# Performance work log

Hardware: AMD Instinct MI355X
Metric: run time of the kernel (lower is better)

Reference implementation:

```python
import jax, jax.numpy as jnp
import numpy as np

N_PDE = 4096
SENSOR_RANGE = 0.08
WINDOW = int(SENSOR_RANGE * N_PDE)   # 327
HALF = WINDOW // 2                   # 163
RESIZE_LEN = 20
FREQS = jnp.array([1.0, 2.0, 4.0, 8.0], dtype=jnp.float32)
EPS = 1e-6  # flax GroupNorm default epsilon
U_MAX, V_MAX = 40.0, 1.0
N_AGENTS = 262144


def setup_inputs() -> dict:
    key = jax.random.key(0)
    ks = jax.random.split(key, 16)

    def w(k, shape):
        fan_in = shape[0]
        return (jax.random.normal(k, shape, jnp.float32) / np.float32(np.sqrt(fan_in)))

    return {
        "z_curr": jax.random.normal(ks[0], (N_PDE,), jnp.float32),
        "z_target": jax.random.normal(ks[1], (N_PDE,), jnp.float32),
        "xi_curr": jax.random.uniform(ks[2], (N_AGENTS,), jnp.float32),
        # branch net (features=[256,256]), each layer: Dense + GroupNorm(1 group) + tanh
        "bW0": w(ks[3], (2 * RESIZE_LEN, 256)), "bb0": jnp.zeros((256,), jnp.float32),
        "bs0": jnp.ones((256,), jnp.float32), "bB0": jnp.zeros((256,), jnp.float32),
        "bW1": w(ks[4], (256, 256)), "bb1": jnp.zeros((256,), jnp.float32),
        "bs1": jnp.ones((256,), jnp.float32), "bB1": jnp.zeros((256,), jnp.float32),
        # trunk net: 8 -> 32 -> 32
        "tW0": w(ks[5], (8, 32)), "tb0": jnp.zeros((32,), jnp.float32),
        "tW1": w(ks[6], (32, 32)), "tb1": jnp.zeros((32,), jnp.float32),
        # combined head: (256+32) -> 32, then two 32 -> 1 heads
        "cW": w(ks[7], (256 + 32, 32)), "cb": jnp.zeros((32,), jnp.float32),
        "uW": w(ks[8], (32, 1)), "ub": jnp.zeros((1,), jnp.float32),
        "vW": w(ks[9], (32, 1)), "vb": jnp.zeros((1,), jnp.float32),
    }


def _local_obs(padded_error, xi):
    # per-agent dynamic slice + finite-difference gradient + bilinear resize
    center = (xi * (N_PDE - 1)).astype(jnp.int32) + HALF
    start = center - HALF
    p_err = jax.lax.dynamic_slice(padded_error, (start,), (WINDOW,))
    p_grad = jnp.gradient(p_err)
    p_err = jax.image.resize(p_err, (RESIZE_LEN,), method='bilinear')
    p_grad = jax.image.resize(p_grad, (RESIZE_LEN,), method='bilinear')
    return jnp.concatenate([p_err, p_grad])  # [40]


def _groupnorm1(x, scale, bias):
    # GroupNorm(num_groups=1) applied per-sample over the feature axis
    mu = jnp.mean(x, axis=-1, keepdims=True)
    var = jnp.var(x, axis=-1, keepdims=True)
    return (x - mu) * jax.lax.rsqrt(var + EPS) * scale + bias


def reference(z_curr, z_target, xi_curr,
              bW0, bb0, bs0, bB0, bW1, bb1, bs1, bB1,
              tW0, tb0, tW1, tb1, cW, cb, uW, ub, vW, vb):
    error = z_curr - z_target
    padded = jnp.pad(error, (HALF, HALF), mode='edge')  # [N_PDE + 2*HALF]

    patches = jax.vmap(lambda xi: _local_obs(padded, xi))(xi_curr)  # [A, 40]

    # branch net
    h = jnp.tanh(_groupnorm1(patches @ bW0 + bb0, bs0, bB0))  # [A, 256]
    h = jnp.tanh(_groupnorm1(h @ bW1 + bb1, bs1, bB1))        # [A, 256]

    # trunk net
    angle = xi_curr[:, None] * FREQS * jnp.pi                 # [A, 4]
    enc = jnp.concatenate([jnp.sin(angle), jnp.cos(angle)], axis=-1)  # [A, 8]
    enc = jnp.tanh(enc @ tW0 + tb0)
    enc = jnp.tanh(enc @ tW1 + tb1)                           # [A, 32]

    combined = jnp.concatenate([h, enc], axis=-1)             # [A, 288]
    x = jnp.tanh(combined @ cW + cb)                          # [A, 32]
    u_raw = (x @ uW + ub).squeeze(-1)
    v_raw = (x @ vW + vb).squeeze(-1)
    return (U_MAX * jnp.tanh(u_raw), V_MAX * jnp.tanh(v_raw))
```

## Files before the change

### kernel.cpp

```cpp
#include <hip/hip_runtime.h>

#define NP      4096
#define WINDOW  327
#define HALF    163
#define RL      20
#define NA      262144
#define GN_EPS  1e-6f
#define R       4
#define NBLK    (NP / R)
#define NT      512

__device__ __forceinline__ float tanh_fast(float x) {
  float e = __expf(2.0f * x);
  return 1.0f - 2.0f / (e + 1.0f);
}

__device__ __forceinline__ void wave_sum2(float& a, float& b) {
#pragma unroll
  for (int m = 1; m < 64; m <<= 1) {
    a += __shfl_xor(a, m, 64);
    b += __shfl_xor(b, m, 64);
  }
}

#define L_ESP   0
#define L_OBS   332
#define L_PART  0
#define L_HBUF  8192
#define L_HCL   9232
#define L_TOT   9376

__global__ __launch_bounds__(NT, 8) void dc_table(
    const float* __restrict__ zc,  const float* __restrict__ zt,
    const float* __restrict__ bW0, const float* __restrict__ bb0,
    const float* __restrict__ bs0, const float* __restrict__ bB0,
    const float* __restrict__ bW1, const float* __restrict__ bb1,
    const float* __restrict__ bs1, const float* __restrict__ bB1,
    const float* __restrict__ tW0, const float* __restrict__ tb0,
    const float* __restrict__ tW1, const float* __restrict__ tb1,
    const float* __restrict__ cW,  const float* __restrict__ cb,
    const float* __restrict__ uW,  const float* __restrict__ ub,
    const float* __restrict__ vW,  const float* __restrict__ vb,
    float* __restrict__ tbl)
{
  __shared__ __align__(16) float sm[L_TOT];
  float* espan = sm + L_ESP;
  float* obsT  = sm + L_OBS;
  float* part  = sm + L_PART;
  float* hbuf  = sm + L_HBUF;
  float* hcL   = sm + L_HCL;

  const int tid = threadIdx.x;
  const int w   = tid >> 6;
  const int l   = tid & 63;
  const int s0  = blockIdx.x * R;

  if (tid < WINDOW + R - 1) {
    int c = s0 - HALF + tid;
    c = c < 0 ? 0 : (c > NP - 1 ? NP - 1 : c);
    espan[tid] = zc[c] - zt[c];
  }
  __syncthreads();

  if (tid < R * 2 * RL) {
    const float INV  = (float)WINDOW / (float)RL;
    const float RINV = (float)RL / (float)WINDOW;
    int q = tid % (2 * RL);
    int r = tid / (2 * RL);
    int qq = (q < RL) ? q : q - RL;
    float xs = ((float)qq + 0.5f) * INV - 0.5f;
    int jlo = (int)ceilf(xs - INV);  if (jlo < 0) jlo = 0;
    int jhi = (int)floorf(xs + INV); if (jhi > WINDOW - 1) jhi = WINDOW - 1;
    const float* p = espan + r;
    float wsum = 0.0f, acc = 0.0f;
    for (int j = jlo; j <= jhi; ++j) {
      float wq = 1.0f - fabsf(xs - (float)j) * RINV;
      float v;
      if (q < RL) {
        v = p[j];
      } else {
        v = (j == 0) ? (p[1] - p[0]) :
            (j == WINDOW - 1) ? (p[WINDOW - 1] - p[WINDOW - 2]) :
            0.5f * (p[j + 1] - p[j - 1]);
      }
      wsum += wq;
      acc  += wq * v;
    }
    obsT[q * 4 + r] = acc / wsum;
  }
  __syncthreads();

  float acc[R][4];

#pragma unroll
  for (int r = 0; r < R; ++r) { acc[r][0]=0.f; acc[r][1]=0.f; acc[r][2]=0.f; acc[r][3]=0.f; }
  for (int kk = 0; kk < 5; ++kk) {
    int k = w * 5 + kk;
    float4 wt = *(const float4*)&bW0[k * 256 + 4 * l];
    float4 o  = *(const float4*)&obsT[k * 4];
    const float wv[4] = {wt.x, wt.y, wt.z, wt.w};
    const float ov[4] = {o.x, o.y, o.z, o.w};
#pragma unroll
    for (int r = 0; r < R; ++r)
#pragma unroll
      for (int j = 0; j < 4; ++j) acc[r][j] = fmaf(ov[r], wv[j], acc[r][j]);
  }
  __syncthreads();

#pragma unroll
  for (int r = 0; r < R; ++r)
    *(float4*)&part[w * 1024 + r * 256 + 4 * l] = make_float4(acc[r][0], acc[r][1], acc[r][2], acc[r][3]);
  __syncthreads();
  if (w < 4) {
    int rr = w, g = l;
    float4 b0 = *(const float4*)&bb0[4 * g];
    float val[4] = {b0.x, b0.y, b0.z, b0.w};
#pragma unroll
    for (int w2 = 0; w2 < 8; ++w2) {
      float4 p0 = *(const float4*)&part[w2 * 1024 + rr * 256 + 4 * g];
      val[0]+=p0.x; val[1]+=p0.y; val[2]+=p0.z; val[3]+=p0.w;
    }
    float s = 0.f, q = 0.f;
#pragma unroll
    for (int i = 0; i < 4; ++i) { s += val[i]; q += val[i] * val[i]; }
    wave_sum2(s, q);
    float mu  = s * (1.0f / 256.0f);
    float var = fmaxf(q * (1.0f / 256.0f) - mu * mu, 0.0f);
    float rv  = rsqrtf(var + GN_EPS);
    float4 sc0 = *(const float4*)&bs0[4 * g];
    float4 sh0 = *(const float4*)&bB0[4 * g];
    const float sc[4] = {sc0.x,sc0.y,sc0.z,sc0.w};
    const float sh[4] = {sh0.x,sh0.y,sh0.z,sh0.w};
    float h[4];
#pragma unroll
    for (int i = 0; i < 4; ++i) h[i] = tanh_fast((val[i] - mu) * rv * sc[i] + sh[i]);
    *(float4*)&hbuf[rr * 260 + 4 * g] = make_float4(h[0], h[1], h[2], h[3]);
  }
  __syncthreads();

#pragma unroll
  for (int r = 0; r < R; ++r) { acc[r][0]=0.f; acc[r][1]=0.f; acc[r][2]=0.f; acc[r][3]=0.f; }
  for (int kk = 0; kk < 32; kk += 4) {
    int k0 = w * 32 + kk;
    float4 wt0 = *(const float4*)&bW1[(k0    ) * 256 + 4 * l];
    float4 wt1 = *(const float4*)&bW1[(k0 + 1) * 256 + 4 * l];
    float4 wt2 = *(const float4*)&bW1[(k0 + 2) * 256 + 4 * l];
    float4 wt3 = *(const float4*)&bW1[(k0 + 3) * 256 + 4 * l];
    float4 hr[R];
#pragma unroll
    for (int r = 0; r < R; ++r) hr[r] = *(const float4*)&hbuf[r * 260 + k0];
#pragma unroll
    for (int r = 0; r < R; ++r) {
      const float* hp = (const float*)&hr[r];
      acc[r][0] = fmaf(hp[0], wt0.x, acc[r][0]); acc[r][1] = fmaf(hp[0], wt0.y, acc[r][1]);
      acc[r][2] = fmaf(hp[0], wt0.z, acc[r][2]); acc[r][3] = fmaf(hp[0], wt0.w, acc[r][3]);
      acc[r][0] = fmaf(hp[1], wt1.x, acc[r][0]); acc[r][1] = fmaf(hp[1], wt1.y, acc[r][1]);
      acc[r][2] = fmaf(hp[1], wt1.z, acc[r][2]); acc[r][3] = fmaf(hp[1], wt1.w, acc[r][3]);
      acc[r][0] = fmaf(hp[2], wt2.x, acc[r][0]); acc[r][1] = fmaf(hp[2], wt2.y, acc[r][1]);
      acc[r][2] = fmaf(hp[2], wt2.z, acc[r][2]); acc[r][3] = fmaf(hp[2], wt2.w, acc[r][3]);
      acc[r][0] = fmaf(hp[3], wt3.x, acc[r][0]); acc[r][1] = fmaf(hp[3], wt3.y, acc[r][1]);
      acc[r][2] = fmaf(hp[3], wt3.z, acc[r][2]); acc[r][3] = fmaf(hp[3], wt3.w, acc[r][3]);
    }
  }

#pragma unroll
  for (int r = 0; r < R; ++r)
    *(float4*)&part[w * 1024 + r * 256 + 4 * l] = make_float4(acc[r][0], acc[r][1], acc[r][2], acc[r][3]);
  __syncthreads();
  if (w < 4) {
    int rr = w, g = l;
    float4 b0 = *(const float4*)&bb1[4 * g];
    float val[4] = {b0.x, b0.y, b0.z, b0.w};
#pragma unroll
    for (int w2 = 0; w2 < 8; ++w2) {
      float4 p0 = *(const float4*)&part[w2 * 1024 + rr * 256 + 4 * g];
      val[0]+=p0.x; val[1]+=p0.y; val[2]+=p0.z; val[3]+=p0.w;
    }
    float s = 0.f, q = 0.f;
#pragma unroll
    for (int i = 0; i < 4; ++i) { s += val[i]; q += val[i] * val[i]; }
    wave_sum2(s, q);
    float mu  = s * (1.0f / 256.0f);
    float var = fmaxf(q * (1.0f / 256.0f) - mu * mu, 0.0f);
    float rv  = rsqrtf(var + GN_EPS);
    float4 sc0 = *(const float4*)&bs1[4 * g];
    float4 sh0 = *(const float4*)&bB1[4 * g];
    const float sc[4] = {sc0.x,sc0.y,sc0.z,sc0.w};
    const float sh[4] = {sh0.x,sh0.y,sh0.z,sh0.w};
    float h[4];
#pragma unroll
    for (int i = 0; i < 4; ++i) h[i] = tanh_fast((val[i] - mu) * rv * sc[i] + sh[i]);
    *(float4*)&hbuf[rr * 260 + 4 * g] = make_float4(h[0], h[1], h[2], h[3]);
  }
  __syncthreads();

  if (w < 4) {
    int r  = w;
    int kg = l >> 3;
    int c  = (l & 7) * 4;
    float ga0 = 0.f, ga1 = 0.f, ga2 = 0.f, ga3 = 0.f;
#pragma unroll
    for (int ii = 0; ii < 8; ++ii) {
      int j  = (ii + kg) & 7;
      int kb = kg * 32 + 4 * j;
      float4 hv = *(const float4*)&hbuf[r * 260 + kb];
      const float hvv[4] = {hv.x, hv.y, hv.z, hv.w};
#pragma unroll
      for (int i2 = 0; i2 < 4; ++i2) {
        float4 cw = *(const float4*)&cW[(kb + i2) * 32 + c];
        ga0 = fmaf(hvv[i2], cw.x, ga0);
        ga1 = fmaf(hvv[i2], cw.y, ga1);
        ga2 = fmaf(hvv[i2], cw.z, ga2);
        ga3 = fmaf(hvv[i2], cw.w, ga3);
      }
    }
#pragma unroll
    for (int m = 8; m < 64; m <<= 1) {
      ga0 += __shfl_xor(ga0, m, 64);
      ga1 += __shfl_xor(ga1, m, 64);
      ga2 += __shfl_xor(ga2, m, 64);
      ga3 += __shfl_xor(ga3, m, 64);
    }
    if (l < 8) {
      float4 cbv = *(const float4*)&cb[c];
      *(float4*)&hcL[r * 36 + c] = make_float4(ga0 + cbv.x, ga1 + cbv.y, ga2 + cbv.z, ga3 + cbv.w);
    }
  }
  __syncthreads();

  if (tid < 64) {
    int v = tid >> 3, sub = tid & 7;
    int r = v >> 1, e = v & 1;
    int jg = s0 + r + e;
    float xe = (float)jg * (1.0f / 4095.0f);
    float enc[8];
#pragma unroll
    for (int k = 0; k < 4; ++k) {
      float fr = (float)(1 << k);
      float a = (xe * fr) * 3.14159265358979f;
      enc[k]     = sinf(a);
      enc[k + 4] = cosf(a);
    }
    int base = tid & ~7;

    float t0v[4];
#pragma unroll
    for (int i = 0; i < 4; ++i) {
      int f = 4 * sub + i;
      float a = tb0[f];
#pragma unroll
      for (int k = 0; k < 8; ++k) a = fmaf(enc[k], tW0[k * 32 + f], a);
      t0v[i] = tanh_fast(a);
    }

    float t1v[4];
#pragma unroll
    for (int i = 0; i < 4; ++i) t1v[i] = tb1[4 * sub + i];
#pragma unroll
    for (int j8 = 0; j8 < 8; ++j8) {
#pragma unroll
      for (int i2 = 0; i2 < 4; ++i2) {
        float tv = __shfl(t0v[i2], base + j8, 64);
        int k = 4 * j8 + i2;
#pragma unroll
        for (int i = 0; i < 4; ++i) t1v[i] = fmaf(tv, tW1[k * 32 + 4 * sub + i], t1v[i]);
      }
    }
#pragma unroll
    for (int i = 0; i < 4; ++i) t1v[i] = tanh_fast(t1v[i]);

    float xvv[4];
#pragma unroll
    for (int i = 0; i < 4; ++i) xvv[i] = hcL[r * 36 + 4 * sub + i];
#pragma unroll
    for (int j8 = 0; j8 < 8; ++j8) {
#pragma unroll
      for (int i2 = 0; i2 < 4; ++i2) {
        float tv = __shfl(t1v[i2], base + j8, 64);
        int k = 4 * j8 + i2;
#pragma unroll
        for (int i = 0; i < 4; ++i) xvv[i] = fmaf(tv, cW[(256 + k) * 32 + 4 * sub + i], xvv[i]);
      }
    }
#pragma unroll
    for (int i = 0; i < 4; ++i) xvv[i] = tanh_fast(xvv[i]);

    float up = 0.f, vp = 0.f;
#pragma unroll
    for (int i = 0; i < 4; ++i) {
      up = fmaf(xvv[i], uW[4 * sub + i], up);
      vp = fmaf(xvv[i], vW[4 * sub + i], vp);
    }
#pragma unroll
    for (int m = 1; m < 8; m <<= 1) {
      up += __shfl_xor(up, m, 64);
      vp += __shfl_xor(vp, m, 64);
    }
    if (sub == 0) {
      int s = s0 + r;
      tbl[4 * s + e]     = 40.0f * tanh_fast(up + ub[0]);
      tbl[4 * s + 2 + e] = tanh_fast(vp + vb[0]);
    }
  }
}

__global__ __launch_bounds__(256) void dc_agents(
    const float* __restrict__ xi_curr, const float4* __restrict__ tbl,
    float* __restrict__ out)
{
  int a = blockIdx.x * 256 + threadIdx.x;
  float xi = xi_curr[a];
  float p = xi * 4095.0f;
  int s = (int)p;
  s = s > 4095 ? 4095 : s;
  float t = p - (float)s;
  float4 tb = tbl[s];
  out[a]      = fmaf(t, tb.y - tb.x, tb.x);
  out[NA + a] = fmaf(t, tb.w - tb.z, tb.z);
}

extern "C" void kernel_launch(void* const* d_in, const int* in_sizes, int n_in,
                              void* d_out, int out_size, void* d_ws, size_t ws_size,
                              hipStream_t stream) {
  const float* zc  = (const float*)d_in[0];
  const float* zt  = (const float*)d_in[1];
  const float* xi  = (const float*)d_in[2];
  const float* bW0 = (const float*)d_in[3];
  const float* bb0 = (const float*)d_in[4];
  const float* bs0 = (const float*)d_in[5];
  const float* bB0 = (const float*)d_in[6];
  const float* bW1 = (const float*)d_in[7];
  const float* bb1 = (const float*)d_in[8];
  const float* bs1 = (const float*)d_in[9];
  const float* bB1 = (const float*)d_in[10];
  const float* tW0 = (const float*)d_in[11];
  const float* tb0 = (const float*)d_in[12];
  const float* tW1 = (const float*)d_in[13];
  const float* tb1 = (const float*)d_in[14];
  const float* cW  = (const float*)d_in[15];
  const float* cb  = (const float*)d_in[16];
  const float* uW  = (const float*)d_in[17];
  const float* ub  = (const float*)d_in[18];
  const float* vW  = (const float*)d_in[19];
  const float* vb  = (const float*)d_in[20];

  float* tbl = (float*)d_ws;
  float* out = (float*)d_out;

  dc_table<<<NBLK, NT, 0, stream>>>(zc, zt, bW0, bb0, bs0, bB0,
                                    bW1, bb1, bs1, bB1,
                                    tW0, tb0, tW1, tb1, cW, cb,
                                    uW, ub, vW, vb, tbl);
  dc_agents<<<NA / 256, 256, 0, stream>>>(xi, (const float4*)tbl, out);
}
```

Before: 146.0 us.

## Process eight table rows per block with 256 threads to improve weight reuse

Doubles the rows handled per block from four to eight and halves the block size to four waves. Each loaded weight vector of the branch-net layers is now reused across eight rows, and the cross-wave reduction is done in two passes of four rows through a smaller shared buffer. The grid halves to 512 blocks, trading block count and register pressure (eight-row accumulators, launch bound of 3) for fewer global weight loads per row.

```diff
diff --git a/kernel.cpp b/kernel.cpp
--- a/kernel.cpp
+++ b/kernel.cpp
@@ -6,9 +6,9 @@
 #define RL      20
 #define NA      262144
 #define GN_EPS  1e-6f
-#define R       4
+#define R       8
 #define NBLK    (NP / R)
-#define NT      512
+#define NT      256
 
 __device__ __forceinline__ float tanh_fast(float x) {
   float e = __expf(2.0f * x);
@@ -24,13 +24,13 @@
 }
 
 #define L_ESP   0
-#define L_OBS   332
+#define L_OBS   336
 #define L_PART  0
-#define L_HBUF  8192
-#define L_HCL   9232
-#define L_TOT   9376
-
-__global__ __launch_bounds__(NT, 8) void dc_table(
+#define L_HBUF  4096
+#define L_HCL   6176
+#define L_TOT   6464
+
+__global__ __launch_bounds__(NT, 3) void dc_table(
     const float* __restrict__ zc,  const float* __restrict__ zt,
     const float* __restrict__ bW0, const float* __restrict__ bb0,
     const float* __restrict__ bs0, const float* __restrict__ bB0,
@@ -55,38 +55,40 @@
   const int l   = tid & 63;
   const int s0  = blockIdx.x * R;
 
-  if (tid < WINDOW + R - 1) {
-    int c = s0 - HALF + tid;
+  for (int t = tid; t < WINDOW + R - 1; t += NT) {
+    int c = s0 - HALF + t;
     c = c < 0 ? 0 : (c > NP - 1 ? NP - 1 : c);
-    espan[tid] = zc[c] - zt[c];
+    espan[t] = zc[c] - zt[c];
   }
   __syncthreads();
 
-  if (tid < R * 2 * RL) {
+  {
     const float INV  = (float)WINDOW / (float)RL;
     const float RINV = (float)RL / (float)WINDOW;
-    int q = tid % (2 * RL);
-    int r = tid / (2 * RL);
-    int qq = (q < RL) ? q : q - RL;
-    float xs = ((float)qq + 0.5f) * INV - 0.5f;
-    int jlo = (int)ceilf(xs - INV);  if (jlo < 0) jlo = 0;
-    int jhi = (int)floorf(xs + INV); if (jhi > WINDOW - 1) jhi = WINDOW - 1;
-    const float* p = espan + r;
-    float wsum = 0.0f, acc = 0.0f;
-    for (int j = jlo; j <= jhi; ++j) {
-      float wq = 1.0f - fabsf(xs - (float)j) * RINV;
-      float v;
-      if (q < RL) {
-        v = p[j];
-      } else {
-        v = (j == 0) ? (p[1] - p[0]) :
-            (j == WINDOW - 1) ? (p[WINDOW - 1] - p[WINDOW - 2]) :
-            0.5f * (p[j + 1] - p[j - 1]);
-      }
-      wsum += wq;
-      acc  += wq * v;
-    }
-    obsT[q * 4 + r] = acc / wsum;
+    for (int task = tid; task < R * 2 * RL; task += NT) {
+      int q = task % (2 * RL);
+      int r = task / (2 * RL);
+      int qq = (q < RL) ? q : q - RL;
+      float xs = ((float)qq + 0.5f) * INV - 0.5f;
+      int jlo = (int)ceilf(xs - INV);  if (jlo < 0) jlo = 0;
+      int jhi = (int)floorf(xs + INV); if (jhi > WINDOW - 1) jhi = WINDOW - 1;
+      const float* p = espan + r;
+      float wsum = 0.0f, acc = 0.0f;
+      for (int j = jlo; j <= jhi; ++j) {
+        float wq = 1.0f - fabsf(xs - (float)j) * RINV;
+        float v;
+        if (q < RL) {
+          v = p[j];
+        } else {
+          v = (j == 0) ? (p[1] - p[0]) :
+              (j == WINDOW - 1) ? (p[WINDOW - 1] - p[WINDOW - 2]) :
+              0.5f * (p[j + 1] - p[j - 1]);
+        }
+        wsum += wq;
+        acc  += wq * v;
+      }
+      obsT[q * 8 + r] = acc / wsum;
+    }
   }
   __syncthreads();
 
@@ -94,12 +96,13 @@
 
 #pragma unroll
   for (int r = 0; r < R; ++r) { acc[r][0]=0.f; acc[r][1]=0.f; acc[r][2]=0.f; acc[r][3]=0.f; }
-  for (int kk = 0; kk < 5; ++kk) {
-    int k = w * 5 + kk;
+  for (int kk = 0; kk < 10; ++kk) {
+    int k = w * 10 + kk;
     float4 wt = *(const float4*)&bW0[k * 256 + 4 * l];
-    float4 o  = *(const float4*)&obsT[k * 4];
+    float4 o0 = *(const float4*)&obsT[k * 8];
+    float4 o1 = *(const float4*)&obsT[k * 8 + 4];
     const float wv[4] = {wt.x, wt.y, wt.z, wt.w};
-    const float ov[4] = {o.x, o.y, o.z, o.w};
+    const float ov[8] = {o0.x, o0.y, o0.z, o0.w, o1.x, o1.y, o1.z, o1.w};
 #pragma unroll
     for (int r = 0; r < R; ++r)
 #pragma unroll
@@ -108,94 +111,106 @@
   __syncthreads();
 
 #pragma unroll
-  for (int r = 0; r < R; ++r)
-    *(float4*)&part[w * 1024 + r * 256 + 4 * l] = make_float4(acc[r][0], acc[r][1], acc[r][2], acc[r][3]);
-  __syncthreads();
-  if (w < 4) {
-    int rr = w, g = l;
-    float4 b0 = *(const float4*)&bb0[4 * g];
-    float val[4] = {b0.x, b0.y, b0.z, b0.w};
-#pragma unroll
-    for (int w2 = 0; w2 < 8; ++w2) {
-      float4 p0 = *(const float4*)&part[w2 * 1024 + rr * 256 + 4 * g];
-      val[0]+=p0.x; val[1]+=p0.y; val[2]+=p0.z; val[3]+=p0.w;
-    }
-    float s = 0.f, q = 0.f;
-#pragma unroll
-    for (int i = 0; i < 4; ++i) { s += val[i]; q += val[i] * val[i]; }
-    wave_sum2(s, q);
-    float mu  = s * (1.0f / 256.0f);
-    float var = fmaxf(q * (1.0f / 256.0f) - mu * mu, 0.0f);
-    float rv  = rsqrtf(var + GN_EPS);
-    float4 sc0 = *(const float4*)&bs0[4 * g];
-    float4 sh0 = *(const float4*)&bB0[4 * g];
-    const float sc[4] = {sc0.x,sc0.y,sc0.z,sc0.w};
-    const float sh[4] = {sh0.x,sh0.y,sh0.z,sh0.w};
-    float h[4];
-#pragma unroll
-    for (int i = 0; i < 4; ++i) h[i] = tanh_fast((val[i] - mu) * rv * sc[i] + sh[i]);
-    *(float4*)&hbuf[rr * 260 + 4 * g] = make_float4(h[0], h[1], h[2], h[3]);
-  }
-  __syncthreads();
+  for (int p = 0; p < 2; ++p) {
+#pragma unroll
+    for (int r = 0; r < 4; ++r)
+      *(float4*)&part[w * 1024 + r * 256 + 4 * l] =
+        make_float4(acc[4*p+r][0], acc[4*p+r][1], acc[4*p+r][2], acc[4*p+r][3]);
+    __syncthreads();
+    {
+      int row = 4 * p + w;
+      float4 b0 = *(const float4*)&bb0[4 * l];
+      float val[4] = {b0.x, b0.y, b0.z, b0.w};
+#pragma unroll
+      for (int w2 = 0; w2 < 4; ++w2) {
+        float4 p0 = *(const float4*)&part[w2 * 1024 + w * 256 + 4 * l];
+        val[0]+=p0.x; val[1]+=p0.y; val[2]+=p0.z; val[3]+=p0.w;
+      }
+      float s = 0.f, q = 0.f;
+#pragma unroll
+      for (int i = 0; i < 4; ++i) { s += val[i]; q += val[i] * val[i]; }
+      wave_sum2(s, q);
+      float mu  = s * (1.0f / 256.0f);
+      float var = fmaxf(q * (1.0f / 256.0f) - mu * mu, 0.0f);
+      float rv  = rsqrtf(var + GN_EPS);
+      float4 sc0 = *(const float4*)&bs0[4 * l];
+      float4 sh0 = *(const float4*)&bB0[4 * l];
+      const float sc[4] = {sc0.x,sc0.y,sc0.z,sc0.w};
+      const float sh[4] = {sh0.x,sh0.y,sh0.z,sh0.w};
+      float h[4];
+#pragma unroll
+      for (int i = 0; i < 4; ++i) h[i] = tanh_fast((val[i] - mu) * rv * sc[i] + sh[i]);
+      *(float4*)&hbuf[row * 260 + 4 * l] = make_float4(h[0], h[1], h[2], h[3]);
+    }
+    __syncthreads();
+  }
 
 #pragma unroll
   for (int r = 0; r < R; ++r) { acc[r][0]=0.f; acc[r][1]=0.f; acc[r][2]=0.f; acc[r][3]=0.f; }
-  for (int kk = 0; kk < 32; kk += 4) {
-    int k0 = w * 32 + kk;
-    float4 wt0 = *(const float4*)&bW1[(k0    ) * 256 + 4 * l];
-    float4 wt1 = *(const float4*)&bW1[(k0 + 1) * 256 + 4 * l];
-    float4 wt2 = *(const float4*)&bW1[(k0 + 2) * 256 + 4 * l];
-    float4 wt3 = *(const float4*)&bW1[(k0 + 3) * 256 + 4 * l];
-    float4 hr[R];
-#pragma unroll
-    for (int r = 0; r < R; ++r) hr[r] = *(const float4*)&hbuf[r * 260 + k0];
-#pragma unroll
-    for (int r = 0; r < R; ++r) {
-      const float* hp = (const float*)&hr[r];
-      acc[r][0] = fmaf(hp[0], wt0.x, acc[r][0]); acc[r][1] = fmaf(hp[0], wt0.y, acc[r][1]);
-      acc[r][2] = fmaf(hp[0], wt0.z, acc[r][2]); acc[r][3] = fmaf(hp[0], wt0.w, acc[r][3]);
-      acc[r][0] = fmaf(hp[1], wt1.x, acc[r][0]); acc[r][1] = fmaf(hp[1], wt1.y, acc[r][1]);
-      acc[r][2] = fmaf(hp[1], wt1.z, acc[r][2]); acc[r][3] = fmaf(hp[1], wt1.w, acc[r][3]);
-      acc[r][0] = fmaf(hp[2], wt2.x, acc[r][0]); acc[r][1] = fmaf(hp[2], wt2.y, acc[r][1]);
-      acc[r][2] = fmaf(hp[2], wt2.z, acc[r][2]); acc[r][3] = fmaf(hp[2], wt2.w, acc[r][3]);
-      acc[r][0] = fmaf(hp[3], wt3.x, acc[r][0]); acc[r][1] = fmaf(hp[3], wt3.y, acc[r][1]);
-      acc[r][2] = fmaf(hp[3], wt3.z, acc[r][2]); acc[r][3] = fmaf(hp[3], wt3.w, acc[r][3]);
-    }
-  }
-
-#pragma unroll
-  for (int r = 0; r < R; ++r)
-    *(float4*)&part[w * 1024 + r * 256 + 4 * l] = make_float4(acc[r][0], acc[r][1], acc[r][2], acc[r][3]);
-  __syncthreads();
-  if (w < 4) {
-    int rr = w, g = l;
-    float4 b0 = *(const float4*)&bb1[4 * g];
-    float val[4] = {b0.x, b0.y, b0.z, b0.w};
-#pragma unroll
-    for (int w2 = 0; w2 < 8; ++w2) {
-      float4 p0 = *(const float4*)&part[w2 * 1024 + rr * 256 + 4 * g];
-      val[0]+=p0.x; val[1]+=p0.y; val[2]+=p0.z; val[3]+=p0.w;
-    }
-    float s = 0.f, q = 0.f;
-#pragma unroll
-    for (int i = 0; i < 4; ++i) { s += val[i]; q += val[i] * val[i]; }
-    wave_sum2(s, q);
-    float mu  = s * (1.0f / 256.0f);
-    float var = fmaxf(q * (1.0f / 256.0f) - mu * mu, 0.0f);
-    float rv  = rsqrtf(var + GN_EPS);
-    float4 sc0 = *(const float4*)&bs1[4 * g];
-    float4 sh0 = *(const float4*)&bB1[4 * g];
-    const float sc[4] = {sc0.x,sc0.y,sc0.z,sc0.w};
-    const float sh[4] = {sh0.x,sh0.y,sh0.z,sh0.w};
-    float h[4];
-#pragma unroll
-    for (int i = 0; i < 4; ++i) h[i] = tanh_fast((val[i] - mu) * rv * sc[i] + sh[i]);
-    *(float4*)&hbuf[rr * 260 + 4 * g] = make_float4(h[0], h[1], h[2], h[3]);
-  }
-  __syncthreads();
-
-  if (w < 4) {
-    int r  = w;
+  for (int kk = 0; kk < 64; kk += 8) {
+    int k0 = w * 64 + kk;
+    float4 wt[8];
+#pragma unroll
+    for (int j = 0; j < 8; ++j) wt[j] = *(const float4*)&bW1[(k0 + j) * 256 + 4 * l];
+#pragma unroll
+    for (int half = 0; half < 2; ++half) {
+      int kb = k0 + 4 * half;
+      float4 hr[R];
+#pragma unroll
+      for (int r = 0; r < R; ++r) hr[r] = *(const float4*)&hbuf[r * 260 + kb];
+#pragma unroll
+      for (int r = 0; r < R; ++r) {
+        const float* hp = (const float*)&hr[r];
+#pragma unroll
+        for (int j = 0; j < 4; ++j) {
+          const float4& wv = wt[4 * half + j];
+          acc[r][0] = fmaf(hp[j], wv.x, acc[r][0]);
+          acc[r][1] = fmaf(hp[j], wv.y, acc[r][1]);
+          acc[r][2] = fmaf(hp[j], wv.z, acc[r][2]);
+          acc[r][3] = fmaf(hp[j], wv.w, acc[r][3]);
+        }
+      }
+    }
+  }
+
+#pragma unroll
+  for (int p = 0; p < 2; ++p) {
+#pragma unroll
+    for (int r = 0; r < 4; ++r)
+      *(float4*)&part[w * 1024 + r * 256 + 4 * l] =
+        make_float4(acc[4*p+r][0], acc[4*p+r][1], acc[4*p+r][2], acc[4*p+r][3]);
+    __syncthreads();
+    {
+      int row = 4 * p + w;
+      float4 b0 = *(const float4*)&bb1[4 * l];
+      float val[4] = {b0.x, b0.y, b0.z, b0.w};
+#pragma unroll
+      for (int w2 = 0; w2 < 4; ++w2) {
+        float4 p0 = *(const float4*)&part[w2 * 1024 + w * 256 + 4 * l];
+        val[0]+=p0.x; val[1]+=p0.y; val[2]+=p0.z; val[3]+=p0.w;
+      }
+      float s = 0.f, q = 0.f;
+#pragma unroll
+      for (int i = 0; i < 4; ++i) { s += val[i]; q += val[i] * val[i]; }
+      wave_sum2(s, q);
+      float mu  = s * (1.0f / 256.0f);
+      float var = fmaxf(q * (1.0f / 256.0f) - mu * mu, 0.0f);
+      float rv  = rsqrtf(var + GN_EPS);
+      float4 sc0 = *(const float4*)&bs1[4 * l];
+      float4 sh0 = *(const float4*)&bB1[4 * l];
+      const float sc[4] = {sc0.x,sc0.y,sc0.z,sc0.w};
+      const float sh[4] = {sh0.x,sh0.y,sh0.z,sh0.w};
+      float h[4];
+#pragma unroll
+      for (int i = 0; i < 4; ++i) h[i] = tanh_fast((val[i] - mu) * rv * sc[i] + sh[i]);
+      *(float4*)&hbuf[row * 260 + 4 * l] = make_float4(h[0], h[1], h[2], h[3]);
+    }
+    __syncthreads();
+  }
+
+#pragma unroll
+  for (int rp = 0; rp < 2; ++rp) {
+    int r  = w + 4 * rp;
     int kg = l >> 3;
     int c  = (l & 7) * 4;
     float ga0 = 0.f, ga1 = 0.f, ga2 = 0.f, ga3 = 0.f;
@@ -228,7 +243,7 @@
   }
   __syncthreads();
 
-  if (tid < 64) {
+  if (tid < 128) {
     int v = tid >> 3, sub = tid & 7;
     int r = v >> 1, e = v & 1;
     int jg = s0 + r + e;
@@ -241,7 +256,7 @@
       enc[k]     = sinf(a);
       enc[k + 4] = cosf(a);
     }
-    int base = tid & ~7;
+    int base = (tid & 63) & ~7;
 
     float t0v[4];
 #pragma unroll
```

After: 129.2 us. -11.5%, faster.

## Process eight grid samples per block and parallelize resize over lane groups

Applied to the files above, without the earlier changes.

Doubles the number of table sample points handled per block from four to eight, so every weight load from bW0/bW1/cW is reused across more rows and all eight waves do work in the GroupNorm and head stages. The bilinear-resize reduction is also split across 8-lane groups with shuffle reductions instead of one serial thread per output. This halves the block count and doubles LDS use and accumulator registers, and the launch-bounds occupancy hint drops from 8 to 4.

```diff
diff --git a/kernel.cpp b/kernel.cpp
--- a/kernel.cpp
+++ b/kernel.cpp
@@ -6,7 +6,7 @@
 #define RL      20
 #define NA      262144
 #define GN_EPS  1e-6f
-#define R       4
+#define R       8
 #define NBLK    (NP / R)
 #define NT      512
 
@@ -24,13 +24,13 @@
 }
 
 #define L_ESP   0
-#define L_OBS   332
+#define L_OBS   336
 #define L_PART  0
-#define L_HBUF  8192
-#define L_HCL   9232
-#define L_TOT   9376
-
-__global__ __launch_bounds__(NT, 8) void dc_table(
+#define L_HBUF  16384
+#define L_HCL   18464
+#define L_TOT   18752
+
+__global__ __launch_bounds__(NT, 4) void dc_table(
     const float* __restrict__ zc,  const float* __restrict__ zt,
     const float* __restrict__ bW0, const float* __restrict__ bb0,
     const float* __restrict__ bs0, const float* __restrict__ bB0,
@@ -62,31 +62,42 @@
   }
   __syncthreads();
 
-  if (tid < R * 2 * RL) {
+  {
     const float INV  = (float)WINDOW / (float)RL;
     const float RINV = (float)RL / (float)WINDOW;
-    int q = tid % (2 * RL);
-    int r = tid / (2 * RL);
-    int qq = (q < RL) ? q : q - RL;
-    float xs = ((float)qq + 0.5f) * INV - 0.5f;
-    int jlo = (int)ceilf(xs - INV);  if (jlo < 0) jlo = 0;
-    int jhi = (int)floorf(xs + INV); if (jhi > WINDOW - 1) jhi = WINDOW - 1;
-    const float* p = espan + r;
-    float wsum = 0.0f, acc = 0.0f;
-    for (int j = jlo; j <= jhi; ++j) {
-      float wq = 1.0f - fabsf(xs - (float)j) * RINV;
-      float v;
-      if (q < RL) {
-        v = p[j];
-      } else {
-        v = (j == 0) ? (p[1] - p[0]) :
-            (j == WINDOW - 1) ? (p[WINDOW - 1] - p[WINDOW - 2]) :
-            0.5f * (p[j + 1] - p[j - 1]);
-      }
-      wsum += wq;
-      acc  += wq * v;
-    }
-    obsT[q * 4 + r] = acc / wsum;
+    const int sub = tid & 7;
+    const int g8  = tid >> 3;
+#pragma unroll
+    for (int it = 0; it < 5; ++it) {
+      int task = it * 64 + g8;
+      int q = task % (2 * RL);
+      int r = task / (2 * RL);
+      int qq = (q < RL) ? q : q - RL;
+      float xs = ((float)qq + 0.5f) * INV - 0.5f;
+      int jlo = (int)ceilf(xs - INV);  if (jlo < 0) jlo = 0;
+      int jhi = (int)floorf(xs + INV); if (jhi > WINDOW - 1) jhi = WINDOW - 1;
+      const float* p = espan + r;
+      float wsum = 0.0f, vsum = 0.0f;
+      for (int j = jlo + sub; j <= jhi; j += 8) {
+        float wq = 1.0f - fabsf(xs - (float)j) * RINV;
+        float v;
+        if (q < RL) {
+          v = p[j];
+        } else {
+          v = (j == 0) ? (p[1] - p[0]) :
+              (j == WINDOW - 1) ? (p[WINDOW - 1] - p[WINDOW - 2]) :
+              0.5f * (p[j + 1] - p[j - 1]);
+        }
+        wsum += wq;
+        vsum += wq * v;
+      }
+#pragma unroll
+      for (int m = 1; m < 8; m <<= 1) {
+        wsum += __shfl_xor(wsum, m, 64);
+        vsum += __shfl_xor(vsum, m, 64);
+      }
+      if (sub == 0) obsT[q * 8 + r] = vsum / wsum;
+    }
   }
   __syncthreads();
 
@@ -97,9 +108,10 @@
   for (int kk = 0; kk < 5; ++kk) {
     int k = w * 5 + kk;
     float4 wt = *(const float4*)&bW0[k * 256 + 4 * l];
-    float4 o  = *(const float4*)&obsT[k * 4];
+    float4 o0 = *(const float4*)&obsT[k * 8];
+    float4 o1 = *(const float4*)&obsT[k * 8 + 4];
     const float wv[4] = {wt.x, wt.y, wt.z, wt.w};
-    const float ov[4] = {o.x, o.y, o.z, o.w};
+    const float ov[8] = {o0.x, o0.y, o0.z, o0.w, o1.x, o1.y, o1.z, o1.w};
 #pragma unroll
     for (int r = 0; r < R; ++r)
 #pragma unroll
@@ -109,15 +121,14 @@
 
 #pragma unroll
   for (int r = 0; r < R; ++r)
-    *(float4*)&part[w * 1024 + r * 256 + 4 * l] = make_float4(acc[r][0], acc[r][1], acc[r][2], acc[r][3]);
-  __syncthreads();
-  if (w < 4) {
-    int rr = w, g = l;
-    float4 b0 = *(const float4*)&bb0[4 * g];
+    *(float4*)&part[w * 2048 + r * 256 + 4 * l] = make_float4(acc[r][0], acc[r][1], acc[r][2], acc[r][3]);
+  __syncthreads();
+  {
+    float4 b0 = *(const float4*)&bb0[4 * l];
     float val[4] = {b0.x, b0.y, b0.z, b0.w};
 #pragma unroll
     for (int w2 = 0; w2 < 8; ++w2) {
-      float4 p0 = *(const float4*)&part[w2 * 1024 + rr * 256 + 4 * g];
+      float4 p0 = *(const float4*)&part[w2 * 2048 + w * 256 + 4 * l];
       val[0]+=p0.x; val[1]+=p0.y; val[2]+=p0.z; val[3]+=p0.w;
     }
     float s = 0.f, q = 0.f;
@@ -127,14 +138,14 @@
     float mu  = s * (1.0f / 256.0f);
     float var = fmaxf(q * (1.0f / 256.0f) - mu * mu, 0.0f);
     float rv  = rsqrtf(var + GN_EPS);
-    float4 sc0 = *(const float4*)&bs0[4 * g];
-    float4 sh0 = *(const float4*)&bB0[4 * g];
+    float4 sc0 = *(const float4*)&bs0[4 * l];
+    float4 sh0 = *(const float4*)&bB0[4 * l];
     const float sc[4] = {sc0.x,sc0.y,sc0.z,sc0.w};
     const float sh[4] = {sh0.x,sh0.y,sh0.z,sh0.w};
     float h[4];
 #pragma unroll
     for (int i = 0; i < 4; ++i) h[i] = tanh_fast((val[i] - mu) * rv * sc[i] + sh[i]);
-    *(float4*)&hbuf[rr * 260 + 4 * g] = make_float4(h[0], h[1], h[2], h[3]);
+    *(float4*)&hbuf[w * 260 + 4 * l] = make_float4(h[0], h[1], h[2], h[3]);
   }
   __syncthreads();
 
@@ -165,15 +176,14 @@
 
 #pragma unroll
   for (int r = 0; r < R; ++r)
-    *(float4*)&part[w * 1024 + r * 256 + 4 * l] = make_float4(acc[r][0], acc[r][1], acc[r][2], acc[r][3]);
-  __syncthreads();
-  if (w < 4) {
-    int rr = w, g = l;
-    float4 b0 = *(const float4*)&bb1[4 * g];
+    *(float4*)&part[w * 2048 + r * 256 + 4 * l] = make_float4(acc[r][0], acc[r][1], acc[r][2], acc[r][3]);
+  __syncthreads();
+  {
+    float4 b0 = *(const float4*)&bb1[4 * l];
     float val[4] = {b0.x, b0.y, b0.z, b0.w};
 #pragma unroll
     for (int w2 = 0; w2 < 8; ++w2) {
-      float4 p0 = *(const float4*)&part[w2 * 1024 + rr * 256 + 4 * g];
+      float4 p0 = *(const float4*)&part[w2 * 2048 + w * 256 + 4 * l];
       val[0]+=p0.x; val[1]+=p0.y; val[2]+=p0.z; val[3]+=p0.w;
     }
     float s = 0.f, q = 0.f;
@@ -183,18 +193,18 @@
     float mu  = s * (1.0f / 256.0f);
     float var = fmaxf(q * (1.0f / 256.0f) - mu * mu, 0.0f);
     float rv  = rsqrtf(var + GN_EPS);
-    float4 sc0 = *(const float4*)&bs1[4 * g];
-    float4 sh0 = *(const float4*)&bB1[4 * g];
+    float4 sc0 = *(const float4*)&bs1[4 * l];
+    float4 sh0 = *(const float4*)&bB1[4 * l];
     const float sc[4] = {sc0.x,sc0.y,sc0.z,sc0.w};
     const float sh[4] = {sh0.x,sh0.y,sh0.z,sh0.w};
     float h[4];
 #pragma unroll
     for (int i = 0; i < 4; ++i) h[i] = tanh_fast((val[i] - mu) * rv * sc[i] + sh[i]);
-    *(float4*)&hbuf[rr * 260 + 4 * g] = make_float4(h[0], h[1], h[2], h[3]);
-  }
-  __syncthreads();
-
-  if (w < 4) {
+    *(float4*)&hbuf[w * 260 + 4 * l] = make_float4(h[0], h[1], h[2], h[3]);
+  }
+  __syncthreads();
+
+  {
     int r  = w;
     int kg = l >> 3;
     int c  = (l & 7) * 4;
@@ -228,7 +238,7 @@
   }
   __syncthreads();
 
-  if (tid < 64) {
+  if (tid < 128) {
     int v = tid >> 3, sub = tid & 7;
     int r = v >> 1, e = v & 1;
     int jg = s0 + r + e;
@@ -241,7 +251,7 @@
       enc[k]     = sinf(a);
       enc[k + 4] = cosf(a);
     }
-    int base = tid & ~7;
+    int base = (tid & 63) & ~7;
 
     float t0v[4];
 #pragma unroll
```

After: 122.8 us. 1.19x faster.
